# Optimization experiments

Measured on AMD Instinct MI355X. Metric: run time of the kernel, lower is better.

The kernel has to match this reference:

```python
import jax, jax.numpy as jnp
import numpy as np

NUM_FORMULAS = 256
NUM_CONJ_ARR = [6, 9, 12, 15]
DEPTH_ARR = [2, 4, 6]
TEMPERATURE = 2.0
INPUT_DIM = 512
BATCH = 8192

# --- static DNF structure (mirrors build-time indicator matrices) ---
_group = NUM_FORMULAS // len(NUM_CONJ_ARR)                       # 64 formulas per group
_conj_per_formula = np.repeat(np.array(NUM_CONJ_ARR), _group)     # [F]
_CONJ2FORM = np.repeat(np.arange(NUM_FORMULAS), _conj_per_formula)  # [C] = 2688
TOTAL_CONJ = int(_CONJ2FORM.shape[0])
_depths = np.tile(np.array(DEPTH_ARR), TOTAL_CONJ // len(DEPTH_ARR))  # depth per conjunction
_LIT2CONJ = np.repeat(np.arange(TOTAL_CONJ), _depths)             # [L] = 10752
TOTAL_LIT = int(_LIT2CONJ.shape[0])


def setup_inputs() -> dict:
    key = jax.random.key(0)
    k = jax.random.split(key, 6)
    x = jax.random.normal(k[0], (BATCH, INPUT_DIM), jnp.float32)
    # literals_random_mask: binary feature-subset mask per literal (build-time constant)
    random_mask = (jax.random.uniform(k[1], (INPUT_DIM, TOTAL_LIT)) < 0.5).astype(jnp.float32)
    glorot = jnp.sqrt(2.0 / (INPUT_DIM + TOTAL_LIT))
    # weight is pre-multiplied by the random mask at build time
    weight = jax.random.normal(k[2], (INPUT_DIM, TOTAL_LIT), jnp.float32) * glorot * random_mask
    # learnable_binary_mask: soft binary-threshold output in [0, 1]
    learnable_binary_mask = jax.random.uniform(k[3], (INPUT_DIM, TOTAL_LIT), jnp.float32)
    bias = jnp.zeros((TOTAL_LIT,), jnp.float32)
    mu = jax.random.normal(k[4], (NUM_FORMULAS, INPUT_DIM), jnp.float32)
    sigma = 1.0 + 0.1 * jax.random.uniform(k[5], (NUM_FORMULAS,), jnp.float32)
    return {
        "x": x, "weight": weight, "learnable_binary_mask": learnable_binary_mask,
        "bias": bias, "mu": mu, "sigma": sigma,
        "lit2conj": jnp.asarray(_LIT2CONJ, jnp.int32),
        "conj2form": jnp.asarray(_CONJ2FORM, jnp.int32),
    }


def reference(x, weight, learnable_binary_mask, bias, mu, sigma, lit2conj, conj2form):
    # literal projection: tanh(x @ (W * M) + b)             -> [B, L]
    literals = jnp.tanh(x @ (weight * learnable_binary_mask) + bias)
    # soft AND over literals of each conjunction: tanh(sum - d + 1.5)
    and_bias = jax.ops.segment_sum(jnp.ones((TOTAL_LIT,), literals.dtype), lit2conj,
                                   num_segments=TOTAL_CONJ)
    conj_sum = jax.ops.segment_sum(literals.T, lit2conj, num_segments=TOTAL_CONJ).T  # [B, C]
    conj = jnp.tanh(conj_sum - and_bias + 1.5)
    # soft OR over conjunctions of each formula: tanh(sum + d - 1.5)
    or_bias = jax.ops.segment_sum(jnp.ones((TOTAL_CONJ,), conj.dtype), conj2form,
                                  num_segments=NUM_FORMULAS)
    form_sum = jax.ops.segment_sum(conj.T, conj2form, num_segments=NUM_FORMULAS).T   # [B, F]
    dnnf = jnp.tanh(form_sum + or_bias - 1.5)
    # localization: softmax over formulas of temperature-scaled RBF, via GEMM expansion
    sq = (jnp.sum(x * x, axis=1, keepdims=True) - 2.0 * (x @ mu.T)
          + jnp.sum(mu * mu, axis=1)[None, :])                                       # [B, F]
    loc = jax.nn.softmax(TEMPERATURE * jnp.exp(-0.5 * sq / (sigma * sigma)[None, :]), axis=-1)
    return dnnf * loc
```

## Files before the change

### kernel.cpp

```cpp
#include <hip/hip_runtime.h>


#define BATCH 8192
#define IDIM 512
#define NFORM 256
#define NLIT 10752
#define WT_ROWS 11136

#define BM 128
#define BN 192
#define BK 32
#define ABYTES 8192
#define BUFB 20480
#define SLITP 196

typedef __bf16 bf16x8 __attribute__((ext_vector_type(8)));
typedef float f32x4 __attribute__((ext_vector_type(4)));
typedef unsigned short u16;
typedef unsigned int u32;

__device__ __forceinline__ u16 f2bf(float f) {
  u32 u = __float_as_uint(f);
  u = (u + 0x7fffu + ((u >> 16) & 1u)) >> 16;
  return (u16)u;
}

__device__ __forceinline__ float fast_tanh(float x) {
  float e = __expf(2.0f * x);
  return 1.0f - 2.0f * __builtin_amdgcn_rcpf(e + 1.0f);
}

__device__ __forceinline__ void async_cp16(const void* g, void* l) {
  __builtin_amdgcn_global_load_lds(
      (const u32 __attribute__((address_space(1)))*)g,
      (u32 __attribute__((address_space(3)))*)l, 16, 0, 0);
}


#define PREPX_BLKS 2048
#define PREPW_BLKS 1344

__global__ __launch_bounds__(256) void prep_all(
    const float* __restrict__ x, const float* __restrict__ W,
    const float* __restrict__ M, const float* __restrict__ mu,
    u16* __restrict__ xb, u16* __restrict__ wt, float* __restrict__ xsq,
    float* __restrict__ musq, float* __restrict__ form_sum) {
  __shared__ float lds[64 * 65];
  const int blk = blockIdx.x, tid = threadIdx.x;

  if (blk < PREPX_BLKS) {
    ((uint4*)form_sum)[blk * 256 + tid] = make_uint4(0, 0, 0, 0);
    int wave = tid >> 6, lane = tid & 63;
    int row = blk * 4 + wave;
    const float4* px = (const float4*)(x + (size_t)row * IDIM);
    float4 a = px[lane * 2], b = px[lane * 2 + 1];
    uint4 pk;
    pk.x = (u32)f2bf(a.x) | ((u32)f2bf(a.y) << 16);
    pk.y = (u32)f2bf(a.z) | ((u32)f2bf(a.w) << 16);
    pk.z = (u32)f2bf(b.x) | ((u32)f2bf(b.y) << 16);
    pk.w = (u32)f2bf(b.z) | ((u32)f2bf(b.w) << 16);
    ((uint4*)(xb + (size_t)row * IDIM))[lane] = pk;
    float s = a.x * a.x + a.y * a.y + a.z * a.z + a.w * a.w +
              b.x * b.x + b.y * b.y + b.z * b.z + b.w * b.w;
#pragma unroll
    for (int o = 32; o > 0; o >>= 1) s += __shfl_down(s, o);
    if (lane == 0) xsq[row] = s;
  } else if (blk < PREPX_BLKS + PREPW_BLKS) {
    int b = blk - PREPX_BLKS;
    int l0 = (b % 168) * 64, k0 = (b / 168) * 64;
#pragma unroll
    for (int j = 0; j < 4; ++j) {
      int idx = tid + j * 256;
      int kk = idx >> 4, l4 = idx & 15;
      size_t g = (size_t)(k0 + kk) * NLIT + l0 + l4 * 4;
      float4 w4 = *(const float4*)(W + g);
      float4 m4 = *(const float4*)(M + g);
      lds[kk * 65 + l4 * 4 + 0] = w4.x * m4.x;
      lds[kk * 65 + l4 * 4 + 1] = w4.y * m4.y;
      lds[kk * 65 + l4 * 4 + 2] = w4.z * m4.z;
      lds[kk * 65 + l4 * 4 + 3] = w4.w * m4.w;
    }
    __syncthreads();
    int l = tid >> 2, kq = tid & 3;
    u32 pk[8];
#pragma unroll
    for (int t = 0; t < 8; ++t) {
      u16 lo = f2bf(lds[(kq * 16 + 2 * t) * 65 + l]);
      u16 hi = f2bf(lds[(kq * 16 + 2 * t + 1) * 65 + l]);
      pk[t] = (u32)lo | ((u32)hi << 16);
    }
    u32* dst = (u32*)(wt + (size_t)(l0 + l) * IDIM + k0 + kq * 16);
    ((uint4*)dst)[0] = make_uint4(pk[0], pk[1], pk[2], pk[3]);
    ((uint4*)dst)[1] = make_uint4(pk[4], pk[5], pk[6], pk[7]);
  } else {
    int b = blk - PREPX_BLKS - PREPW_BLKS;
    if (b < 256) {
      float s = 0.f;
#pragma unroll
      for (int j = tid; j < IDIM; j += 256) {
        float v = mu[(size_t)b * IDIM + j];
        wt[(size_t)(NLIT + b) * IDIM + j] = f2bf(v);
        s += v * v;
      }
      float* red = lds;
      red[tid] = s;
      __syncthreads();
      for (int sh = 128; sh > 0; sh >>= 1) {
        if (tid < sh) red[tid] += red[tid + sh];
        __syncthreads();
      }
      if (tid == 0) musq[b] = red[0];
    } else {
      int row = NLIT + 256 + (b - 256);
      for (int j = tid; j < IDIM; j += 256) wt[(size_t)row * IDIM + j] = 0;
    }
  }
}


__global__ __launch_bounds__(256, 3) void dnnf_gemm(
    const u16* __restrict__ xb, const u16* __restrict__ wt,
    const float* __restrict__ bias, float* __restrict__ form_sum,
    float* __restrict__ dotbuf) {
  __shared__ __align__(16) char smraw[2 * BUFB];
  float* slit = (float*)smraw;

  const int tid = threadIdx.x;
  const int wave = tid >> 6, lane = tid & 63;
  const int wm = wave & 1, wn = wave >> 1;
  const int m0 = blockIdx.x * BM, n0 = blockIdx.y * BN;
  const int q = lane >> 4, cn = lane & 15;

  const int kgs = ((tid & 3) ^ ((tid >> 2) & 3) ^ ((tid >> 4) & 3)) * 8;
  const u16* pa = xb + (size_t)(m0 + (tid >> 2)) * IDIM + kgs;
  const u16* pb = wt + (size_t)(n0 + (tid >> 2)) * IDIM + kgs;
  const int dA = tid * 16;
  const int dB = ABYTES + tid * 16;

  const int swz16 = (q ^ (cn & 3) ^ ((cn >> 2) & 3)) << 4;
  int offA[4], offB[6];
#pragma unroll
  for (int mf = 0; mf < 4; ++mf)
    offA[mf] = (wm * 64 + mf * 16 + cn) * 64 + swz16;
#pragma unroll
  for (int nf = 0; nf < 6; ++nf)
    offB[nf] = ABYTES + (wn * 96 + nf * 16 + cn) * 64 + swz16;

  f32x4 acc[4][6];
#pragma unroll
  for (int a = 0; a < 4; ++a)
#pragma unroll
    for (int b = 0; b < 6; ++b) acc[a][b] = (f32x4){0.f, 0.f, 0.f, 0.f};

#pragma unroll
  for (int i = 0; i < 2; ++i)
    async_cp16(pa + (size_t)i * 64 * IDIM, smraw + dA + i * 4096);
#pragma unroll
  for (int i = 0; i < 3; ++i)
    async_cp16(pb + (size_t)i * 64 * IDIM, smraw + dB + i * 4096);
  pa += BK;
  pb += BK;

#pragma unroll
  for (int kt = 0; kt < 16; ++kt) {
    const char* bufc = smraw + (kt & 1) * BUFB;
    if (kt < 15) {
      char* bufn = smraw + ((kt + 1) & 1) * BUFB;
#pragma unroll
      for (int i = 0; i < 2; ++i)
        async_cp16(pa + (size_t)i * 64 * IDIM, bufn + dA + i * 4096);
#pragma unroll
      for (int i = 0; i < 3; ++i)
        async_cp16(pb + (size_t)i * 64 * IDIM, bufn + dB + i * 4096);
      pa += BK;
      pb += BK;
      asm volatile("s_waitcnt vmcnt(5)\n\ts_barrier" ::: "memory");
    } else {
      asm volatile("s_waitcnt vmcnt(0)\n\ts_barrier" ::: "memory");
    }
    bf16x8 af[4], bfr[6];
#pragma unroll
    for (int mf = 0; mf < 4; ++mf)
      af[mf] = *(const bf16x8*)(bufc + offA[mf]);
#pragma unroll
    for (int nf = 0; nf < 6; ++nf)
      bfr[nf] = *(const bf16x8*)(bufc + offB[nf]);
#pragma unroll
    for (int mf = 0; mf < 4; ++mf)
#pragma unroll
      for (int nf = 0; nf < 6; ++nf)
        acc[mf][nf] = __builtin_amdgcn_mfma_f32_16x16x32_bf16(
            af[mf], bfr[nf], acc[mf][nf], 0, 0, 0);
    if (kt < 15)
      asm volatile("s_waitcnt lgkmcnt(0)\n\ts_barrier" ::: "memory");
  }
  __syncthreads();

  if (n0 < NLIT) {
    float bv[6];
#pragma unroll
    for (int nf = 0; nf < 6; ++nf) bv[nf] = bias[n0 + wn * 96 + nf * 16 + cn];

#pragma unroll
    for (int ph = 0; ph < 4; ++ph) {
      if (ph) __syncthreads();
      if (wm == (ph >> 1)) {
#pragma unroll
        for (int mh = 0; mh < 2; ++mh) {
          int mf = 2 * (ph & 1) + mh;
#pragma unroll
          for (int nf = 0; nf < 6; ++nf) {
            int col = wn * 96 + nf * 16 + cn;
#pragma unroll
            for (int reg = 0; reg < 4; ++reg) {
              int sr = mh * 16 + q * 4 + reg;
              slit[sr * SLITP + col] = fast_tanh(acc[mf][nf][reg] + bv[nf]);
            }
          }
        }
      }
      __syncthreads();

      int r = tid >> 3, sub = tid & 7;
      const float* lrow = slit + r * SLITP + sub * 24;
      int c0 = ((n0 + sub * 24) / 12) * 3;
      size_t grow = (size_t)(m0 + ph * 32 + r) * NFORM;
      float run = 0.f;
      int fprev = -1;
#pragma unroll
      for (int tr = 0; tr < 2; ++tr) {
        const float4 a0 = *(const float4*)(lrow + tr * 12);
        const float4 a1 = *(const float4*)(lrow + tr * 12 + 4);
        const float4 a2 = *(const float4*)(lrow + tr * 12 + 8);
        float s2 = a0.x + a0.y;
        float s4 = a0.z + a0.w + a1.x + a1.y;
        float s6 = a1.z + a1.w + a2.x + a2.y + a2.z + a2.w;
        float v = fast_tanh(s2 - 0.5f) + fast_tanh(s4 - 2.5f) +
                  fast_tanh(s6 - 4.5f);
        int c = c0 + tr * 3;
        int f = (c < 384)    ? (c / 6)
                : (c < 960)  ? 64 + (c - 384) / 9
                : (c < 1728) ? 128 + (c - 960) / 12
                             : 192 + (c - 1728) / 15;
        if (f != fprev) {
          if (fprev >= 0) atomicAdd(form_sum + grow + fprev, run);
          fprev = f;
          run = 0.f;
        }
        run += v;
      }
      atomicAdd(form_sum + grow + fprev, run);
    }
  } else {
#pragma unroll
    for (int nf = 0; nf < 6; ++nf) {
      int col = n0 - NLIT + wn * 96 + nf * 16 + cn;
      if (col < NFORM) {
#pragma unroll
        for (int mf = 0; mf < 4; ++mf)
#pragma unroll
          for (int reg = 0; reg < 4; ++reg) {
            int row = wm * 64 + mf * 16 + q * 4 + reg;
            dotbuf[(size_t)(m0 + row) * NFORM + col] = acc[mf][nf][reg];
          }
      }
    }
  }
}


__global__ __launch_bounds__(256) void finale(
    const float* __restrict__ form_sum, const float* __restrict__ dotbuf,
    const float* __restrict__ xsq, const float* __restrict__ musq,
    const float* __restrict__ sigma, float* __restrict__ out) {
  int wave = threadIdx.x >> 6, lane = threadIdx.x & 63;
  int r = blockIdx.x * 4 + wave;
  size_t base = (size_t)r * NFORM;
  float xs = xsq[r];
  float e[4], s = 0.f;
#pragma unroll
  for (int j = 0; j < 4; ++j) {
    int f = j * 64 + lane;
    float sq = xs - 2.0f * dotbuf[base + f] + musq[f];
    float sg = sigma[f];
    float p = __expf(-0.5f * sq / (sg * sg));
    e[j] = __expf(2.0f * p);
    s += e[j];
  }
#pragma unroll
  for (int o = 32; o > 0; o >>= 1) s += __shfl_xor(s, o);
  float inv = __builtin_amdgcn_rcpf(s);
#pragma unroll
  for (int j = 0; j < 4; ++j) {
    int f = j * 64 + lane;
    float dn = fast_tanh(form_sum[base + f] + (float)(6 + 3 * j) - 1.5f);
    out[base + f] = dn * e[j] * inv;
  }
}


extern "C" void kernel_launch(void* const* d_in, const int* in_sizes, int n_in,
                              void* d_out, int out_size, void* d_ws,
                              size_t ws_size, hipStream_t stream) {
  const float* x = (const float*)d_in[0];
  const float* W = (const float*)d_in[1];
  const float* M = (const float*)d_in[2];
  const float* bias = (const float*)d_in[3];
  const float* mu = (const float*)d_in[4];
  const float* sigma = (const float*)d_in[5];
  float* out = (float*)d_out;

  float* form_sum = (float*)d_ws;
  float* dotbuf = form_sum + (size_t)BATCH * NFORM;
  u16* xb = (u16*)(dotbuf + (size_t)BATCH * NFORM);
  u16* wt = xb + (size_t)BATCH * IDIM;
  float* xsq = (float*)(wt + (size_t)WT_ROWS * IDIM);
  float* musq = xsq + BATCH;

  prep_all<<<PREPX_BLKS + PREPW_BLKS + 384, 256, 0, stream>>>(
      x, W, M, mu, xb, wt, xsq, musq, form_sum);
  dnnf_gemm<<<dim3(BATCH / BM, WT_ROWS / BN), 256, 0, stream>>>(xb, wt, bias,
                                                                form_sum, dotbuf);
  finale<<<BATCH / 4, 256, 0, stream>>>(form_sum, dotbuf, xsq, musq, sigma, out);
}
```

Baseline: 237.5 us.

## Load GEMM B fragments directly from global into registers, bypassing LDS

```diff
diff --git a/kernel.cpp b/kernel.cpp
--- a/kernel.cpp
+++ b/kernel.cpp
@@ -10,8 +10,7 @@
 #define BM 128
 #define BN 192
 #define BK 32
-#define ABYTES 8192
-#define BUFB 20480
+#define ABUF 8192
 #define SLITP 196
 
 typedef __bf16 bf16x8 __attribute__((ext_vector_type(8)));
@@ -122,100 +121,93 @@
     const u16* __restrict__ xb, const u16* __restrict__ wt,
     const float* __restrict__ bias, float* __restrict__ form_sum,
     float* __restrict__ dotbuf) {
-  __shared__ __align__(16) char smraw[2 * BUFB];
+  __shared__ __align__(16) char smraw[25088];
   float* slit = (float*)smraw;
 
   const int tid = threadIdx.x;
   const int wave = tid >> 6, lane = tid & 63;
-  const int wm = wave & 1, wn = wave >> 1;
+  const int wn = wave;
   const int m0 = blockIdx.x * BM, n0 = blockIdx.y * BN;
   const int q = lane >> 4, cn = lane & 15;
 
   const int kgs = ((tid & 3) ^ ((tid >> 2) & 3) ^ ((tid >> 4) & 3)) * 8;
   const u16* pa = xb + (size_t)(m0 + (tid >> 2)) * IDIM + kgs;
-  const u16* pb = wt + (size_t)(n0 + (tid >> 2)) * IDIM + kgs;
   const int dA = tid * 16;
-  const int dB = ABYTES + tid * 16;
 
   const int swz16 = (q ^ (cn & 3) ^ ((cn >> 2) & 3)) << 4;
-  int offA[4], offB[6];
-#pragma unroll
-  for (int mf = 0; mf < 4; ++mf)
-    offA[mf] = (wm * 64 + mf * 16 + cn) * 64 + swz16;
-#pragma unroll
-  for (int nf = 0; nf < 6; ++nf)
-    offB[nf] = ABYTES + (wn * 96 + nf * 16 + cn) * 64 + swz16;
-
-  f32x4 acc[4][6];
-#pragma unroll
-  for (int a = 0; a < 4; ++a)
-#pragma unroll
-    for (int b = 0; b < 6; ++b) acc[a][b] = (f32x4){0.f, 0.f, 0.f, 0.f};
+  int offA[8];
+#pragma unroll
+  for (int mf = 0; mf < 8; ++mf) offA[mf] = (mf * 16 + cn) * 64 + swz16;
+
+  const u16* pbr[3];
+#pragma unroll
+  for (int nf = 0; nf < 3; ++nf)
+    pbr[nf] = wt + (size_t)(n0 + wn * 48 + nf * 16 + cn) * IDIM + q * 8;
+
+  f32x4 acc[8][3];
+#pragma unroll
+  for (int a = 0; a < 8; ++a)
+#pragma unroll
+    for (int b = 0; b < 3; ++b) acc[a][b] = (f32x4){0.f, 0.f, 0.f, 0.f};
+
+  bf16x8 bfr[2][3];
 
 #pragma unroll
   for (int i = 0; i < 2; ++i)
     async_cp16(pa + (size_t)i * 64 * IDIM, smraw + dA + i * 4096);
 #pragma unroll
-  for (int i = 0; i < 3; ++i)
-    async_cp16(pb + (size_t)i * 64 * IDIM, smraw + dB + i * 4096);
-  pa += BK;
-  pb += BK;
+  for (int nf = 0; nf < 3; ++nf) bfr[0][nf] = *(const bf16x8*)(pbr[nf]);
 
 #pragma unroll
   for (int kt = 0; kt < 16; ++kt) {
-    const char* bufc = smraw + (kt & 1) * BUFB;
+    const char* bufc = smraw + (kt & 1) * ABUF;
     if (kt < 15) {
-      char* bufn = smraw + ((kt + 1) & 1) * BUFB;
+      char* bufn = smraw + ((kt + 1) & 1) * ABUF;
+#pragma unroll
+      for (int nf = 0; nf < 3; ++nf)
+        bfr[(kt + 1) & 1][nf] =
+            *(const bf16x8*)(pbr[nf] + (size_t)(kt + 1) * BK);
 #pragma unroll
       for (int i = 0; i < 2; ++i)
-        async_cp16(pa + (size_t)i * 64 * IDIM, bufn + dA + i * 4096);
-#pragma unroll
-      for (int i = 0; i < 3; ++i)
-        async_cp16(pb + (size_t)i * 64 * IDIM, bufn + dB + i * 4096);
-      pa += BK;
-      pb += BK;
+        async_cp16(pa + (size_t)i * 64 * IDIM + (kt + 1) * BK,
+                   bufn + dA + i * 4096);
       asm volatile("s_waitcnt vmcnt(5)\n\ts_barrier" ::: "memory");
     } else {
       asm volatile("s_waitcnt vmcnt(0)\n\ts_barrier" ::: "memory");
     }
-    bf16x8 af[4], bfr[6];
-#pragma unroll
-    for (int mf = 0; mf < 4; ++mf)
+    bf16x8 af[8];
+#pragma unroll
+    for (int mf = 0; mf < 8; ++mf)
       af[mf] = *(const bf16x8*)(bufc + offA[mf]);
 #pragma unroll
-    for (int nf = 0; nf < 6; ++nf)
-      bfr[nf] = *(const bf16x8*)(bufc + offB[nf]);
-#pragma unroll
-    for (int mf = 0; mf < 4; ++mf)
-#pragma unroll
-      for (int nf = 0; nf < 6; ++nf)
+    for (int mf = 0; mf < 8; ++mf)
+#pragma unroll
+      for (int nf = 0; nf < 3; ++nf)
         acc[mf][nf] = __builtin_amdgcn_mfma_f32_16x16x32_bf16(
-            af[mf], bfr[nf], acc[mf][nf], 0, 0, 0);
+            af[mf], bfr[kt & 1][nf], acc[mf][nf], 0, 0, 0);
     if (kt < 15)
       asm volatile("s_waitcnt lgkmcnt(0)\n\ts_barrier" ::: "memory");
   }
   __syncthreads();
 
   if (n0 < NLIT) {
-    float bv[6];
-#pragma unroll
-    for (int nf = 0; nf < 6; ++nf) bv[nf] = bias[n0 + wn * 96 + nf * 16 + cn];
+    float bv[3];
+#pragma unroll
+    for (int nf = 0; nf < 3; ++nf) bv[nf] = bias[n0 + wn * 48 + nf * 16 + cn];
 
 #pragma unroll
     for (int ph = 0; ph < 4; ++ph) {
       if (ph) __syncthreads();
-      if (wm == (ph >> 1)) {
-#pragma unroll
-        for (int mh = 0; mh < 2; ++mh) {
-          int mf = 2 * (ph & 1) + mh;
-#pragma unroll
-          for (int nf = 0; nf < 6; ++nf) {
-            int col = wn * 96 + nf * 16 + cn;
-#pragma unroll
-            for (int reg = 0; reg < 4; ++reg) {
-              int sr = mh * 16 + q * 4 + reg;
-              slit[sr * SLITP + col] = fast_tanh(acc[mf][nf][reg] + bv[nf]);
-            }
+#pragma unroll
+      for (int mh = 0; mh < 2; ++mh) {
+        int mf = 2 * ph + mh;
+#pragma unroll
+        for (int nf = 0; nf < 3; ++nf) {
+          int col = wn * 48 + nf * 16 + cn;
+#pragma unroll
+          for (int reg = 0; reg < 4; ++reg) {
+            int sr = mh * 16 + q * 4 + reg;
+            slit[sr * SLITP + col] = fast_tanh(acc[mf][nf][reg] + bv[nf]);
           }
         }
       }
@@ -253,14 +245,14 @@
     }
   } else {
 #pragma unroll
-    for (int nf = 0; nf < 6; ++nf) {
-      int col = n0 - NLIT + wn * 96 + nf * 16 + cn;
+    for (int nf = 0; nf < 3; ++nf) {
+      int col = n0 - NLIT + wn * 48 + nf * 16 + cn;
       if (col < NFORM) {
 #pragma unroll
-        for (int mf = 0; mf < 4; ++mf)
+        for (int mf = 0; mf < 8; ++mf)
 #pragma unroll
           for (int reg = 0; reg < 4; ++reg) {
-            int row = wm * 64 + mf * 16 + q * 4 + reg;
+            int row = mf * 16 + q * 4 + reg;
             dotbuf[(size_t)(m0 + row) * NFORM + col] = acc[mf][nf][reg];
           }
       }
```

After: 246.5 us. +3.8%, slower.

## Fuse finale into GEMM via last-block-per-row-tile atomic counter

Applied to the files above, without the earlier changes.

```diff
diff --git a/kernel.cpp b/kernel.cpp
--- a/kernel.cpp
+++ b/kernel.cpp
@@ -6,6 +6,7 @@
 #define NFORM 256
 #define NLIT 10752
 #define WT_ROWS 11136
+#define NTILES 58
 
 #define BM 128
 #define BN 192
@@ -44,11 +45,13 @@
     const float* __restrict__ x, const float* __restrict__ W,
     const float* __restrict__ M, const float* __restrict__ mu,
     u16* __restrict__ xb, u16* __restrict__ wt, float* __restrict__ xsq,
-    float* __restrict__ musq, float* __restrict__ form_sum) {
+    float* __restrict__ musq, float* __restrict__ form_sum,
+    u32* __restrict__ cnt) {
   __shared__ float lds[64 * 65];
   const int blk = blockIdx.x, tid = threadIdx.x;
 
   if (blk < PREPX_BLKS) {
+    if (blk == 0 && tid < 64) cnt[tid] = 0;
     ((uint4*)form_sum)[blk * 256 + tid] = make_uint4(0, 0, 0, 0);
     int wave = tid >> 6, lane = tid & 63;
     int row = blk * 4 + wave;
@@ -121,8 +124,11 @@
 __global__ __launch_bounds__(256, 3) void dnnf_gemm(
     const u16* __restrict__ xb, const u16* __restrict__ wt,
     const float* __restrict__ bias, float* __restrict__ form_sum,
-    float* __restrict__ dotbuf) {
+    float* __restrict__ dotbuf, const float* __restrict__ xsq,
+    const float* __restrict__ musq, const float* __restrict__ sigma,
+    float* __restrict__ out, u32* __restrict__ cnt) {
   __shared__ __align__(16) char smraw[2 * BUFB];
+  __shared__ int slast;
   float* slit = (float*)smraw;
 
   const int tid = threadIdx.x;
@@ -266,35 +272,36 @@
       }
     }
   }
-}
-
-
-__global__ __launch_bounds__(256) void finale(
-    const float* __restrict__ form_sum, const float* __restrict__ dotbuf,
-    const float* __restrict__ xsq, const float* __restrict__ musq,
-    const float* __restrict__ sigma, float* __restrict__ out) {
-  int wave = threadIdx.x >> 6, lane = threadIdx.x & 63;
-  int r = blockIdx.x * 4 + wave;
-  size_t base = (size_t)r * NFORM;
-  float xs = xsq[r];
-  float e[4], s = 0.f;
-#pragma unroll
-  for (int j = 0; j < 4; ++j) {
-    int f = j * 64 + lane;
-    float sq = xs - 2.0f * dotbuf[base + f] + musq[f];
-    float sg = sigma[f];
-    float p = __expf(-0.5f * sq / (sg * sg));
-    e[j] = __expf(2.0f * p);
-    s += e[j];
-  }
-#pragma unroll
-  for (int o = 32; o > 0; o >>= 1) s += __shfl_xor(s, o);
-  float inv = __builtin_amdgcn_rcpf(s);
-#pragma unroll
-  for (int j = 0; j < 4; ++j) {
-    int f = j * 64 + lane;
-    float dn = fast_tanh(form_sum[base + f] + (float)(6 + 3 * j) - 1.5f);
-    out[base + f] = dn * e[j] * inv;
+
+  __threadfence();
+  if (tid == 0) slast = (atomicAdd(&cnt[blockIdx.x], 1u) == NTILES - 1);
+  __syncthreads();
+  if (slast) {
+    __threadfence();
+    const int ln = lane;
+    for (int r8 = wave; r8 < BM; r8 += 4) {
+      size_t base = (size_t)(m0 + r8) * NFORM;
+      float xs = xsq[m0 + r8];
+      float e[4], s = 0.f;
+#pragma unroll
+      for (int j = 0; j < 4; ++j) {
+        int f = j * 64 + ln;
+        float sq = xs - 2.0f * dotbuf[base + f] + musq[f];
+        float sg = sigma[f];
+        float p = __expf(-0.5f * sq / (sg * sg));
+        e[j] = __expf(2.0f * p);
+        s += e[j];
+      }
+#pragma unroll
+      for (int o = 32; o > 0; o >>= 1) s += __shfl_xor(s, o);
+      float inv = __builtin_amdgcn_rcpf(s);
+#pragma unroll
+      for (int j = 0; j < 4; ++j) {
+        int f = j * 64 + ln;
+        float dn = fast_tanh(form_sum[base + f] + (float)(6 + 3 * j) - 1.5f);
+        out[base + f] = dn * e[j] * inv;
+      }
+    }
   }
 }
 
@@ -316,10 +323,10 @@
   u16* wt = xb + (size_t)BATCH * IDIM;
   float* xsq = (float*)(wt + (size_t)WT_ROWS * IDIM);
   float* musq = xsq + BATCH;
+  u32* cnt = (u32*)(musq + NFORM);
 
   prep_all<<<PREPX_BLKS + PREPW_BLKS + 384, 256, 0, stream>>>(
-      x, W, M, mu, xb, wt, xsq, musq, form_sum);
-  dnnf_gemm<<<dim3(BATCH / BM, WT_ROWS / BN), 256, 0, stream>>>(xb, wt, bias,
-                                                                form_sum, dotbuf);
-  finale<<<BATCH / 4, 256, 0, stream>>>(form_sum, dotbuf, xsq, musq, sigma, out);
-}
+      x, W, M, mu, xb, wt, xsq, musq, form_sum, cnt);
+  dnnf_gemm<<<dim3(BATCH / BM, WT_ROWS / BN), 256, 0, stream>>>(
+      xb, wt, bias, form_sum, dotbuf, xsq, musq, sigma, out, cnt);
+}
```

Result: slower. 498.3 us (+109.8%).
